# Kernel tuning notes

Hardware: AMD Instinct MI355X
Metric: run time of the kernel (lower is better)

## Reference

```python
import jax, jax.numpy as jnp
import numpy as np

N_NODES = 100000
N_EDGES = 1000000
D = 64
HID = 64
OUT = 64
N_CLS = 10
N_GRAPHS = 512
BN_EPS = 1e-5


def setup_inputs() -> dict:
    key = jax.random.key(0)
    ks = jax.random.split(key, 16)
    inp = {
        "x": jax.random.normal(ks[0], (N_NODES, D), dtype=jnp.float32),
        "edge_index": jax.random.randint(ks[1], (2, N_EDGES), 0, N_NODES, dtype=jnp.int32),
        "batch": jnp.sort(jax.random.randint(ks[2], (N_NODES,), 0, N_GRAPHS, dtype=jnp.int32)),
    }
    def lin(k, fi, fo):
        lim = 1.0 / np.sqrt(fi)
        kw, kb = jax.random.split(k)
        return (jax.random.uniform(kw, (fi, fo), minval=-lim, maxval=lim, dtype=jnp.float32),
                jax.random.uniform(kb, (fo,), minval=-lim, maxval=lim, dtype=jnp.float32))
    # conv0 MLP([64,64,64]) with BN after first linear
    inp["w0a"], inp["b0a"] = lin(ks[3], D, HID)
    inp["g0"] = jnp.ones((HID,), jnp.float32); inp["be0"] = jnp.zeros((HID,), jnp.float32)
    inp["m0"] = jnp.zeros((HID,), jnp.float32); inp["v0"] = jnp.ones((HID,), jnp.float32)
    inp["w0b"], inp["b0b"] = lin(ks[4], HID, HID)
    # conv1 MLP([64,64,64])
    inp["w1a"], inp["b1a"] = lin(ks[5], HID, HID)
    inp["g1"] = jnp.ones((HID,), jnp.float32); inp["be1"] = jnp.zeros((HID,), jnp.float32)
    inp["m1"] = jnp.zeros((HID,), jnp.float32); inp["v1"] = jnp.ones((HID,), jnp.float32)
    inp["w1b"], inp["b1b"] = lin(ks[6], HID, OUT)
    # classifier
    inp["wc"], inp["bc"] = lin(ks[7], OUT, N_CLS)
    return inp


def _bn_eval(h, g, b, m, v):
    return (h - m) * jax.lax.rsqrt(v + BN_EPS) * g + b


def _mlp(h, wa, ba, g, be, m, v, wb, bb):
    # Linear -> BN -> ReLU -> (dropout eval=identity) -> Linear
    h = h @ wa + ba
    h = jax.nn.relu(_bn_eval(h, g, be, m, v))
    return h @ wb + bb


def _gin_conv(h, src, dst, wa, ba, g, be, m, v, wb, bb):
    # GINConv eps=0: mlp(x + sum_{j->i} x_j), messages scatter-added at dst
    agg = jax.ops.segment_sum(h[src], dst, num_segments=N_NODES)
    return _mlp(h + agg, wa, ba, g, be, m, v, wb, bb)


def reference(x, edge_index, batch,
              w0a, b0a, g0, be0, m0, v0, w0b, b0b,
              w1a, b1a, g1, be1, m1, v1, w1b, b1b,
              wc, bc):
    src, dst = edge_index[0], edge_index[1]
    h = _gin_conv(x, src, dst, w0a, b0a, g0, be0, m0, v0, w0b, b0b)
    h = jax.nn.relu(h)  # dropout is identity in eval
    h = _gin_conv(h, src, dst, w1a, b1a, g1, be1, m1, v1, w1b, b1b)
    # global mean pool over batch indices
    sums = jax.ops.segment_sum(h, batch, num_segments=N_GRAPHS)
    cnts = jax.ops.segment_sum(jnp.ones((h.shape[0],), h.dtype), batch, num_segments=N_GRAPHS)
    pooled = sums / jnp.maximum(cnts, 1.0)[:, None]
    return pooled @ wc + bc
```

## Files before the change

kernel.cpp:

```cpp
#include <hip/hip_runtime.h>

#define N_NODES 100000
#define N_EDGES 1000000
#define N_GRAPHS 512
#define N_CLS 10
#define BN_EPS 1e-5f

#define SCAN_NB 200
#define NTILES2 3125

typedef _Float16 half8 __attribute__((ext_vector_type(8)));
typedef _Float16 half4v __attribute__((ext_vector_type(4)));
typedef float floatx4 __attribute__((ext_vector_type(4)));

__global__ __launch_bounds__(256) void prep_kernel(
    const float* __restrict__ x, _Float16* __restrict__ xh,
    const int* __restrict__ batch, const int* __restrict__ dstI,
    int* __restrict__ deg, int* __restrict__ rank,
    const float* __restrict__ w0a, const float* __restrict__ b0a,
    const float* __restrict__ g0, const float* __restrict__ be0,
    const float* __restrict__ m0, const float* __restrict__ v0,
    const float* __restrict__ w0b,
    const float* __restrict__ w1a, const float* __restrict__ b1a,
    const float* __restrict__ g1, const float* __restrict__ be1,
    const float* __restrict__ m1, const float* __restrict__ v1,
    const float* __restrict__ w1b,
    int* __restrict__ gstart,
    _Float16* __restrict__ wHi, _Float16* __restrict__ wLo,
    float* __restrict__ b1p0, float* __restrict__ b1p1) {
    const int gid = blockIdx.x * 256 + threadIdx.x;

    if (gid < 1600000) {
        float4 v = ((const float4*)x)[gid];
        half4v h = {(_Float16)v.x, (_Float16)v.y, (_Float16)v.z, (_Float16)v.w};
        ((half4v*)xh)[gid] = h;
    }

    if (gid < N_EDGES)
        rank[gid] = atomicAdd(&deg[dstI[gid]], 1);

    if (gid <= N_NODES) {
        int bcur = (gid < N_NODES) ? batch[gid] : N_GRAPHS;
        int bprev = (gid > 0) ? batch[gid - 1] : -1;
        for (int g = bprev + 1; g <= bcur; ++g) gstart[g] = gid;
    }

    if (gid < 16384) {
        const int e = gid & 4095, mat = gid >> 12;
        const int jj = e & 7, lane = (e >> 3) & 63, c = (e >> 9) & 3, k0 = (e >> 11) & 1;
        const int k = k0 * 32 + (lane >> 4) * 8 + jj;
        const int col = c * 16 + (lane & 15);
        float val;
        if (mat == 0)      val = w0a[k * 64 + col] * (rsqrtf(v0[col] + BN_EPS) * g0[col]);
        else if (mat == 1) val = w0b[k * 64 + col];
        else if (mat == 2) val = w1a[k * 64 + col] * (rsqrtf(v1[col] + BN_EPS) * g1[col]);
        else               val = w1b[k * 64 + col];
        _Float16 hi = (_Float16)val;
        wHi[gid] = hi;
        wLo[gid] = (_Float16)(val - (float)hi);
    }

    if (gid >= 16384 && gid < 16512) {
        int t = gid - 16384;
        if (t < 64) {
            float s = rsqrtf(v0[t] + BN_EPS) * g0[t];
            b1p0[t] = (b0a[t] - m0[t]) * s + be0[t];
        } else {
            t -= 64;
            float s = rsqrtf(v1[t] + BN_EPS) * g1[t];
            b1p1[t] = (b1a[t] - m1[t]) * s + be1[t];
        }
    }
}

__global__ __launch_bounds__(256) void scanA_kernel(const int* __restrict__ deg,
                                                    int* __restrict__ bsum) {
    __shared__ int sh[256];
    const int base = blockIdx.x * 512;
    const int t = threadIdx.x;
    int a = 0, b = 0;
    if (base + t < N_NODES) a = deg[base + t];
    if (base + 256 + t < N_NODES) b = deg[base + 256 + t];
    sh[t] = a + b;
    __syncthreads();
#pragma unroll
    for (int off = 128; off > 0; off >>= 1) {
        if (t < off) sh[t] += sh[t + off];
        __syncthreads();
    }
    if (t == 0) bsum[blockIdx.x] = sh[0];
}

__global__ __launch_bounds__(256) void scanC_kernel(const int* __restrict__ deg,
                                                    const int* __restrict__ bsum,
                                                    int* __restrict__ rowptr) {
    __shared__ int sh[256];
    __shared__ int sboff[256];
    const int base = blockIdx.x * 512;
    const int t = threadIdx.x;

    const int bv = (t < SCAN_NB) ? bsum[t] : 0;
    sboff[t] = bv;

    const int i0 = base + 2 * t, i1 = i0 + 1;
    const int d0 = (i0 < N_NODES) ? deg[i0] : 0;
    const int d1 = (i1 < N_NODES) ? deg[i1] : 0;
    const int p = d0 + d1;
    sh[t] = p;
    __syncthreads();
#pragma unroll
    for (int off = 1; off < 256; off <<= 1) {
        int u = (t >= off) ? sh[t - off] : 0;
        int ub = (t >= off) ? sboff[t - off] : 0;
        __syncthreads();
        sh[t] += u;
        sboff[t] += ub;
        __syncthreads();
    }
    const int myoff = (blockIdx.x == 0) ? 0 : sboff[blockIdx.x - 1];
    const int excl = myoff + sh[t] - p;
    if (i0 < N_NODES) rowptr[i0] = excl;
    if (i1 < N_NODES) rowptr[i1] = excl + d0;
    if (blockIdx.x == 0 && t == 0) rowptr[N_NODES] = N_EDGES;
}

__global__ __launch_bounds__(256) void fill_kernel(const int* __restrict__ srcI,
                                                   const int* __restrict__ dstI,
                                                   const int* __restrict__ rank,
                                                   const int* __restrict__ rowptr,
                                                   int* __restrict__ sortedSrc) {
    int e = blockIdx.x * 256 + threadIdx.x;
    if (e >= N_EDGES) return;
    sortedSrc[rowptr[dstI[e]] + rank[e]] = srcI[e];
}

template <int POOL>
__global__ __launch_bounds__(128) void conv_mfma(
    const _Float16* __restrict__ in, const int* __restrict__ rowptr,
    const int* __restrict__ srcList,
    const _Float16* __restrict__ wH1, const _Float16* __restrict__ wL1,
    const _Float16* __restrict__ wH2, const _Float16* __restrict__ wL2,
    const float* __restrict__ b1, const float* __restrict__ b2,
    _Float16* __restrict__ out, const int* __restrict__ batch,
    float* __restrict__ pooled) {
    __shared__ __align__(16) _Float16 scratch[2][2304];
    __shared__ float pooledLoc[8 * 64];
    __shared__ int bIds[32];
    __shared__ int maxSlot;

    const int tid = threadIdx.x;
    const int j = tid & 63, wv = tid >> 6;
    const int eoff = j >> 4;
    const int lf = j & 15;
    const int base = blockIdx.x * 32;
    const int strip0 = base + wv * 16;

    if (POOL) {
#pragma unroll
        for (int q = 0; q < 4; ++q) pooledLoc[tid + q * 128] = 0.f;
        if (tid == 0) maxSlot = 0;
        if (j < 16) bIds[wv * 16 + j] = batch[strip0 + j];
    }

    const int rpv = rowptr[strip0 + min(j, 16)];

    _Float16* aggH = scratch[wv];
    _Float16* aggL = scratch[wv] + 1152;

    for (int mq = 0; mq < 4; ++mq) {
        const int m0 = mq * 4;
        int rr[5];
#pragma unroll
        for (int i = 0; i < 5; ++i) rr[i] = __builtin_amdgcn_readlane(rpv, m0 + i);
        int cnt[4];
#pragma unroll
        for (int i = 0; i < 4; ++i) cnt[i] = rr[i + 1] - rr[i];

        float aR[4][4];
#pragma unroll
        for (int i = 0; i < 4; ++i)
#pragma unroll
            for (int q = 0; q < 4; ++q) aR[i][q] = 0.f;

        half4v sS[4];
#pragma unroll
        for (int i = 0; i < 4; ++i) {
            sS[i] = (half4v){0, 0, 0, 0};
            if (eoff == 0)
                sS[i] = *(const half4v*)(in + (size_t)(strip0 + m0 + i) * 64 + lf * 4);
        }
        half4v vT[4][4];
#pragma unroll
        for (int i = 0; i < 4; ++i) {
            const int g = (min(cnt[i], 16) + 3) >> 2;
#pragma unroll
            for (int k = 0; k < 4; ++k) {
                vT[i][k] = (half4v){0, 0, 0, 0};
                if (k < g) {
                    int ec = min(4 * k + eoff, cnt[i] - 1);
                    int id = srcList[rr[i] + ec];
                    vT[i][k] = *(const half4v*)(in + (size_t)id * 64 + lf * 4);
                }
            }
        }
#pragma unroll
        for (int i = 0; i < 4; ++i) {
#pragma unroll
            for (int k = 0; k < 4; ++k) {
                if (4 * k + eoff < cnt[i]) {
                    aR[i][0] += (float)vT[i][k].x; aR[i][1] += (float)vT[i][k].y;
                    aR[i][2] += (float)vT[i][k].z; aR[i][3] += (float)vT[i][k].w;
                }
            }
        }
#pragma unroll
        for (int i = 0; i < 4; ++i) {
            for (int eb = 16; eb < cnt[i]; eb += 16) {
#pragma unroll
                for (int k = 0; k < 4; ++k) {
                    int e_ = eb + 4 * k + eoff;
                    if (e_ < cnt[i]) {
                        int id = srcList[rr[i] + e_];
                        half4v t = *(const half4v*)(in + (size_t)id * 64 + lf * 4);
                        aR[i][0] += (float)t.x; aR[i][1] += (float)t.y;
                        aR[i][2] += (float)t.z; aR[i][3] += (float)t.w;
                    }
                }
            }
        }
#pragma unroll
        for (int i = 0; i < 4; ++i) {
            if (eoff == 0) {
                aR[i][0] += (float)sS[i].x; aR[i][1] += (float)sS[i].y;
                aR[i][2] += (float)sS[i].z; aR[i][3] += (float)sS[i].w;
            }
#pragma unroll
            for (int q = 0; q < 4; ++q) {
                aR[i][q] += __shfl_xor(aR[i][q], 16, 64);
                aR[i][q] += __shfl_xor(aR[i][q], 32, 64);
            }
            if (j < 16) {
                half4v hi, lo;
#pragma unroll
                for (int q = 0; q < 4; ++q) {
                    hi[q] = (_Float16)aR[i][q];
                    lo[q] = (_Float16)(aR[i][q] - (float)hi[q]);
                }
                *(half4v*)(aggH + (m0 + i) * 72 + 4 * j) = hi;
                *(half4v*)(aggL + (m0 + i) * 72 + 4 * j) = lo;
            }
        }
    }

    const int l15 = j & 15, quad = j >> 4;
    const floatx4 vzero = {0.f, 0.f, 0.f, 0.f};

    floatx4 acc[4] = {vzero, vzero, vzero, vzero};
    {
        const _Float16* aH0 = aggH + l15 * 72 + quad * 8;
        const _Float16* aL0 = aggL + l15 * 72 + quad * 8;
#pragma unroll
        for (int k0 = 0; k0 < 2; ++k0) {
            half8 aH = *(const half8*)(aH0 + k0 * 32);
            half8 aL = *(const half8*)(aL0 + k0 * 32);
#pragma unroll
            for (int c = 0; c < 4; ++c) {
                const int fo = ((k0 * 4 + c) * 64 + j) * 8;
                half8 bH = *(const half8*)(wH1 + fo);
                half8 bL = *(const half8*)(wL1 + fo);
                acc[c] = __builtin_amdgcn_mfma_f32_16x16x32_f16(aH, bH, acc[c], 0, 0, 0);
                acc[c] = __builtin_amdgcn_mfma_f32_16x16x32_f16(aL, bH, acc[c], 0, 0, 0);
                acc[c] = __builtin_amdgcn_mfma_f32_16x16x32_f16(aH, bL, acc[c], 0, 0, 0);
            }
        }
    }
    _Float16* hH = aggH;
    _Float16* hL = aggL;
#pragma unroll
    for (int c = 0; c < 4; ++c) {
        const float bv = b1[c * 16 + l15];
#pragma unroll
        for (int r = 0; r < 4; ++r) {
            const int row = quad * 4 + r, col = c * 16 + l15;
            float v = acc[c][r] + bv;
            v = fmaxf(v, 0.f);
            const _Float16 hi = (_Float16)v;
            hH[row * 72 + col] = hi;
            hL[row * 72 + col] = (_Float16)(v - (float)hi);
        }
    }

    floatx4 acc2[4] = {vzero, vzero, vzero, vzero};
    {
        const _Float16* aH0 = hH + l15 * 72 + quad * 8;
        const _Float16* aL0 = hL + l15 * 72 + quad * 8;
#pragma unroll
        for (int k0 = 0; k0 < 2; ++k0) {
            half8 aH = *(const half8*)(aH0 + k0 * 32);
            half8 aL = *(const half8*)(aL0 + k0 * 32);
#pragma unroll
            for (int c = 0; c < 4; ++c) {
                const int fo = ((k0 * 4 + c) * 64 + j) * 8;
                half8 bH = *(const half8*)(wH2 + fo);
                half8 bL = *(const half8*)(wL2 + fo);
                acc2[c] = __builtin_amdgcn_mfma_f32_16x16x32_f16(aH, bH, acc2[c], 0, 0, 0);
                acc2[c] = __builtin_amdgcn_mfma_f32_16x16x32_f16(aL, bH, acc2[c], 0, 0, 0);
                acc2[c] = __builtin_amdgcn_mfma_f32_16x16x32_f16(aH, bL, acc2[c], 0, 0, 0);
            }
        }
    }

    if (!POOL) {
#pragma unroll
        for (int c = 0; c < 4; ++c) {
            const float bv = b2[c * 16 + l15];
#pragma unroll
            for (int r = 0; r < 4; ++r) {
                const int node = strip0 + quad * 4 + r;
                out[(size_t)node * 64 + c * 16 + l15] =
                    (_Float16)fmaxf(acc2[c][r] + bv, 0.f);
            }
        }
    } else {
        float* oT = (float*)scratch[wv];
#pragma unroll
        for (int c = 0; c < 4; ++c) {
            const float bv = b2[c * 16 + l15];
#pragma unroll
            for (int r = 0; r < 4; ++r)
                oT[(quad * 4 + r) * 66 + c * 16 + l15] = acc2[c][r] + bv;
        }
        __syncthreads();
        const int b0 = bIds[0];
        int curB = -1;
        float accv = 0.f;
        for (int r = 0; r < 16; ++r) {
            const int b = bIds[wv * 16 + r];
            const float v = oT[r * 66 + j];
            if (b != curB) {
                if (curB >= 0) {
                    const int s = curB - b0;
                    if (s >= 0 && s < 8) {
                        atomicAdd(&pooledLoc[s * 64 + j], accv);
                        if (j == 0) atomicMax(&maxSlot, s);
                    } else {
                        atomicAdd(&pooled[curB * 64 + j], accv);
                    }
                }
                curB = b;
                accv = v;
            } else {
                accv += v;
            }
        }
        {
            const int s = curB - b0;
            if (s >= 0 && s < 8) {
                atomicAdd(&pooledLoc[s * 64 + j], accv);
                if (j == 0) atomicMax(&maxSlot, s);
            } else {
                atomicAdd(&pooled[curB * 64 + j], accv);
            }
        }
        __syncthreads();
        const int ns = maxSlot + 1;
        for (int s = wv; s < ns; s += 2)
            atomicAdd(&pooled[(b0 + s) * 64 + j], pooledLoc[s * 64 + j]);
    }
}

__global__ __launch_bounds__(64) void classifier_kernel(const float* __restrict__ pooled,
                                                        const int* __restrict__ gstart,
                                                        const float* __restrict__ wc,
                                                        const float* __restrict__ bc,
                                                        float* __restrict__ out) {
    const int g = blockIdx.x;
    const int j = threadIdx.x;
    const float c = fmaxf((float)(gstart[g + 1] - gstart[g]), 1.f);
    const float mean = pooled[g * 64 + j] / c;
#pragma unroll
    for (int cc = 0; cc < N_CLS; ++cc) {
        float p = mean * wc[j * N_CLS + cc];
#pragma unroll
        for (int off = 32; off > 0; off >>= 1) p += __shfl_down(p, off, 64);
        if (j == 0) out[g * N_CLS + cc] = p + bc[cc];
    }
}


extern "C" void kernel_launch(void* const* d_in, const int* in_sizes, int n_in,
                              void* d_out, int out_size, void* d_ws, size_t ws_size,
                              hipStream_t stream) {
    const float* x   = (const float*)d_in[0];
    const int*   ei  = (const int*)d_in[1];
    const int* batch = (const int*)d_in[2];
    const float* w0a = (const float*)d_in[3];
    const float* b0a = (const float*)d_in[4];
    const float* g0  = (const float*)d_in[5];
    const float* be0 = (const float*)d_in[6];
    const float* m0  = (const float*)d_in[7];
    const float* v0  = (const float*)d_in[8];
    const float* w0b = (const float*)d_in[9];
    const float* b0b = (const float*)d_in[10];
    const float* w1a = (const float*)d_in[11];
    const float* b1a = (const float*)d_in[12];
    const float* g1  = (const float*)d_in[13];
    const float* be1 = (const float*)d_in[14];
    const float* m1  = (const float*)d_in[15];
    const float* v1  = (const float*)d_in[16];
    const float* w1b = (const float*)d_in[17];
    const float* b1b = (const float*)d_in[18];
    const float* wc  = (const float*)d_in[19];
    const float* bc  = (const float*)d_in[20];
    float* out = (float*)d_out;

    const int* srcI = ei;
    const int* dstI = ei + N_EDGES;

    int* ws = (int*)d_ws;
    int*      deg       = ws;
    int*      bsum      = ws + 100000;
    float*    pooled    = (float*)(ws + 100404);
    int*      rowptr    = ws + 133172;
    int*      rank      = ws + 233176;
    int*      sortedSrc = ws + 1233176;
    _Float16* xh        = (_Float16*)(ws + 2233176);
    _Float16* h1        = (_Float16*)(ws + 5433176);
    float*    b1p0      = (float*)(ws + 8633176);
    float*    b1p1      = (float*)(ws + 8633240);
    int*      gstart    = ws + 8633304;
    _Float16* wHi       = (_Float16*)(ws + 8633820);
    _Float16* wLo       = (_Float16*)(ws + 8642012);

    (void)hipMemsetAsync((void*)deg, 0, 133172 * sizeof(int), stream);
    prep_kernel<<<6250, 256, 0, stream>>>(x, xh, batch, dstI, deg, rank,
                                          w0a, b0a, g0, be0, m0, v0, w0b,
                                          w1a, b1a, g1, be1, m1, v1, w1b,
                                          gstart, wHi, wLo, b1p0, b1p1);

    scanA_kernel<<<SCAN_NB, 256, 0, stream>>>(deg, bsum);
    scanC_kernel<<<SCAN_NB, 256, 0, stream>>>(deg, bsum, rowptr);
    fill_kernel<<<(N_EDGES + 255) / 256, 256, 0, stream>>>(srcI, dstI, rank, rowptr, sortedSrc);

    conv_mfma<0><<<NTILES2, 128, 0, stream>>>(xh, rowptr, sortedSrc,
                                              wHi, wLo, wHi + 4096, wLo + 4096,
                                              b1p0, b0b, h1, nullptr, nullptr);

    conv_mfma<1><<<NTILES2, 128, 0, stream>>>(h1, rowptr, sortedSrc,
                                              wHi + 8192, wLo + 8192, wHi + 12288, wLo + 12288,
                                              b1p1, b1b, nullptr, batch, pooled);

    classifier_kernel<<<N_GRAPHS, 64, 0, stream>>>(pooled, gstart, wc, bc, out);
}
```

Baseline: 292.0 us.

## Merge CSR build stages into one cooperative kernel with grid syncs

```diff
diff --git a/kernel.cpp b/kernel.cpp
--- a/kernel.cpp
+++ b/kernel.cpp
@@ -1,4 +1,5 @@
 #include <hip/hip_runtime.h>
+#include <hip/hip_cooperative_groups.h>
 
 #define N_NODES 100000
 #define N_EDGES 1000000
@@ -6,16 +7,19 @@
 #define N_CLS 10
 #define BN_EPS 1e-5f
 
-#define SCAN_NB 200
 #define NTILES2 3125
+#define CB 512
+#define CCHUNK 196
+#define ZN 133172
 
 typedef _Float16 half8 __attribute__((ext_vector_type(8)));
 typedef _Float16 half4v __attribute__((ext_vector_type(4)));
 typedef float floatx4 __attribute__((ext_vector_type(4)));
 
-__global__ __launch_bounds__(256) void prep_kernel(
+__global__ __launch_bounds__(256) void build_kernel(
     const float* __restrict__ x, _Float16* __restrict__ xh,
-    const int* __restrict__ batch, const int* __restrict__ dstI,
+    const int* __restrict__ batch, const int* __restrict__ srcI,
+    const int* __restrict__ dstI,
     int* __restrict__ deg, int* __restrict__ rank,
     const float* __restrict__ w0a, const float* __restrict__ b0a,
     const float* __restrict__ g0, const float* __restrict__ be0,
@@ -27,24 +31,32 @@
     const float* __restrict__ w1b,
     int* __restrict__ gstart,
     _Float16* __restrict__ wHi, _Float16* __restrict__ wLo,
-    float* __restrict__ b1p0, float* __restrict__ b1p1) {
-    const int gid = blockIdx.x * 256 + threadIdx.x;
-
-    if (gid < 1600000) {
-        float4 v = ((const float4*)x)[gid];
+    float* __restrict__ b1p0, float* __restrict__ b1p1,
+    int* __restrict__ bsum, int* __restrict__ boff,
+    int* __restrict__ rowptr, int* __restrict__ sortedSrc) {
+    cooperative_groups::grid_group grid = cooperative_groups::this_grid();
+    __shared__ int sh[256];
+
+    const int t = threadIdx.x;
+    const int blk = blockIdx.x;
+    const int gid = blk * 256 + t;
+    const int stride = CB * 256;
+
+    for (int i = gid; i < ZN; i += stride) deg[i] = 0;
+    grid.sync();
+
+    for (int i = gid; i < 1600000; i += stride) {
+        float4 v = ((const float4*)x)[i];
         half4v h = {(_Float16)v.x, (_Float16)v.y, (_Float16)v.z, (_Float16)v.w};
-        ((half4v*)xh)[gid] = h;
-    }
-
-    if (gid < N_EDGES)
-        rank[gid] = atomicAdd(&deg[dstI[gid]], 1);
-
-    if (gid <= N_NODES) {
-        int bcur = (gid < N_NODES) ? batch[gid] : N_GRAPHS;
-        int bprev = (gid > 0) ? batch[gid - 1] : -1;
-        for (int g = bprev + 1; g <= bcur; ++g) gstart[g] = gid;
-    }
-
+        ((half4v*)xh)[i] = h;
+    }
+    for (int e = gid; e < N_EDGES; e += stride)
+        rank[e] = atomicAdd(&deg[dstI[e]], 1);
+    for (int i = gid; i <= N_NODES; i += stride) {
+        int bcur = (i < N_NODES) ? batch[i] : N_GRAPHS;
+        int bprev = (i > 0) ? batch[i - 1] : -1;
+        for (int g = bprev + 1; g <= bcur; ++g) gstart[g] = i;
+    }
     if (gid < 16384) {
         const int e = gid & 4095, mat = gid >> 12;
         const int jj = e & 7, lane = (e >> 3) & 63, c = (e >> 9) & 3, k0 = (e >> 11) & 1;
@@ -59,79 +71,68 @@
         wHi[gid] = hi;
         wLo[gid] = (_Float16)(val - (float)hi);
     }
-
     if (gid >= 16384 && gid < 16512) {
-        int t = gid - 16384;
-        if (t < 64) {
-            float s = rsqrtf(v0[t] + BN_EPS) * g0[t];
-            b1p0[t] = (b0a[t] - m0[t]) * s + be0[t];
+        int tt = gid - 16384;
+        if (tt < 64) {
+            float s = rsqrtf(v0[tt] + BN_EPS) * g0[tt];
+            b1p0[tt] = (b0a[tt] - m0[tt]) * s + be0[tt];
         } else {
-            t -= 64;
-            float s = rsqrtf(v1[t] + BN_EPS) * g1[t];
-            b1p1[t] = (b1a[t] - m1[t]) * s + be1[t];
-        }
-    }
-}
-
-__global__ __launch_bounds__(256) void scanA_kernel(const int* __restrict__ deg,
-                                                    int* __restrict__ bsum) {
-    __shared__ int sh[256];
-    const int base = blockIdx.x * 512;
-    const int t = threadIdx.x;
-    int a = 0, b = 0;
-    if (base + t < N_NODES) a = deg[base + t];
-    if (base + 256 + t < N_NODES) b = deg[base + 256 + t];
-    sh[t] = a + b;
-    __syncthreads();
-#pragma unroll
-    for (int off = 128; off > 0; off >>= 1) {
-        if (t < off) sh[t] += sh[t + off];
+            tt -= 64;
+            float s = rsqrtf(v1[tt] + BN_EPS) * g1[tt];
+            b1p1[tt] = (b1a[tt] - m1[tt]) * s + be1[tt];
+        }
+    }
+    grid.sync();
+
+    {
+        const int idx = blk * CCHUNK + t;
+        sh[t] = (t < CCHUNK && idx < N_NODES) ? deg[idx] : 0;
         __syncthreads();
-    }
-    if (t == 0) bsum[blockIdx.x] = sh[0];
-}
-
-__global__ __launch_bounds__(256) void scanC_kernel(const int* __restrict__ deg,
-                                                    const int* __restrict__ bsum,
-                                                    int* __restrict__ rowptr) {
-    __shared__ int sh[256];
-    __shared__ int sboff[256];
-    const int base = blockIdx.x * 512;
-    const int t = threadIdx.x;
-
-    const int bv = (t < SCAN_NB) ? bsum[t] : 0;
-    sboff[t] = bv;
-
-    const int i0 = base + 2 * t, i1 = i0 + 1;
-    const int d0 = (i0 < N_NODES) ? deg[i0] : 0;
-    const int d1 = (i1 < N_NODES) ? deg[i1] : 0;
-    const int p = d0 + d1;
-    sh[t] = p;
-    __syncthreads();
-#pragma unroll
-    for (int off = 1; off < 256; off <<= 1) {
-        int u = (t >= off) ? sh[t - off] : 0;
-        int ub = (t >= off) ? sboff[t - off] : 0;
+#pragma unroll
+        for (int off = 128; off > 0; off >>= 1) {
+            if (t < off) sh[t] += sh[t + off];
+            __syncthreads();
+        }
+        if (t == 0) bsum[blk] = sh[0];
+    }
+    grid.sync();
+
+    if (blk == 0) {
+        const int a = bsum[2 * t], b = bsum[2 * t + 1];
+        sh[t] = a + b;
         __syncthreads();
-        sh[t] += u;
-        sboff[t] += ub;
+#pragma unroll
+        for (int off = 1; off < 256; off <<= 1) {
+            int u = (t >= off) ? sh[t - off] : 0;
+            __syncthreads();
+            sh[t] += u;
+            __syncthreads();
+        }
+        const int exclPair = sh[t] - (a + b);
+        boff[2 * t] = exclPair;
+        boff[2 * t + 1] = exclPair + a;
+    }
+    grid.sync();
+
+    {
+        const int idx = blk * CCHUNK + t;
+        const int v = (t < CCHUNK && idx < N_NODES) ? deg[idx] : 0;
+        sh[t] = v;
         __syncthreads();
-    }
-    const int myoff = (blockIdx.x == 0) ? 0 : sboff[blockIdx.x - 1];
-    const int excl = myoff + sh[t] - p;
-    if (i0 < N_NODES) rowptr[i0] = excl;
-    if (i1 < N_NODES) rowptr[i1] = excl + d0;
-    if (blockIdx.x == 0 && t == 0) rowptr[N_NODES] = N_EDGES;
-}
-
-__global__ __launch_bounds__(256) void fill_kernel(const int* __restrict__ srcI,
-                                                   const int* __restrict__ dstI,
-                                                   const int* __restrict__ rank,
-                                                   const int* __restrict__ rowptr,
-                                                   int* __restrict__ sortedSrc) {
-    int e = blockIdx.x * 256 + threadIdx.x;
-    if (e >= N_EDGES) return;
-    sortedSrc[rowptr[dstI[e]] + rank[e]] = srcI[e];
+#pragma unroll
+        for (int off = 1; off < 256; off <<= 1) {
+            int u = (t >= off) ? sh[t - off] : 0;
+            __syncthreads();
+            sh[t] += u;
+            __syncthreads();
+        }
+        if (t < CCHUNK && idx < N_NODES) rowptr[idx] = boff[blk] + sh[t] - v;
+        if (blk == 0 && t == 0) rowptr[N_NODES] = N_EDGES;
+    }
+    grid.sync();
+
+    for (int e = gid; e < N_EDGES; e += stride)
+        sortedSrc[rowptr[dstI[e]] + rank[e]] = srcI[e];
 }
 
 template <int POOL>
@@ -221,9 +222,9 @@
                     int e_ = eb + 4 * k + eoff;
                     if (e_ < cnt[i]) {
                         int id = srcList[rr[i] + e_];
-                        half4v t = *(const half4v*)(in + (size_t)id * 64 + lf * 4);
-                        aR[i][0] += (float)t.x; aR[i][1] += (float)t.y;
-                        aR[i][2] += (float)t.z; aR[i][3] += (float)t.w;
+                        half4v tv = *(const half4v*)(in + (size_t)id * 64 + lf * 4);
+                        aR[i][0] += (float)tv.x; aR[i][1] += (float)tv.y;
+                        aR[i][2] += (float)tv.z; aR[i][3] += (float)tv.w;
                     }
                 }
             }
@@ -420,27 +421,30 @@
     int* ws = (int*)d_ws;
     int*      deg       = ws;
     int*      bsum      = ws + 100000;
-    float*    pooled    = (float*)(ws + 100404);
-    int*      rowptr    = ws + 133172;
-    int*      rank      = ws + 233176;
-    int*      sortedSrc = ws + 1233176;
-    _Float16* xh        = (_Float16*)(ws + 2233176);
-    _Float16* h1        = (_Float16*)(ws + 5433176);
-    float*    b1p0      = (float*)(ws + 8633176);
-    float*    b1p1      = (float*)(ws + 8633240);
-    int*      gstart    = ws + 8633304;
-    _Float16* wHi       = (_Float16*)(ws + 8633820);
-    _Float16* wLo       = (_Float16*)(ws + 8642012);
-
-    (void)hipMemsetAsync((void*)deg, 0, 133172 * sizeof(int), stream);
-    prep_kernel<<<6250, 256, 0, stream>>>(x, xh, batch, dstI, deg, rank,
-                                          w0a, b0a, g0, be0, m0, v0, w0b,
-                                          w1a, b1a, g1, be1, m1, v1, w1b,
-                                          gstart, wHi, wLo, b1p0, b1p1);
-
-    scanA_kernel<<<SCAN_NB, 256, 0, stream>>>(deg, bsum);
-    scanC_kernel<<<SCAN_NB, 256, 0, stream>>>(deg, bsum, rowptr);
-    fill_kernel<<<(N_EDGES + 255) / 256, 256, 0, stream>>>(srcI, dstI, rank, rowptr, sortedSrc);
+    float*    pooled    = (float*)(ws + 100516);
+    int*      boff      = ws + 133284;
+    int*      rowptr    = ws + 133800;
+    int*      rank      = ws + 233804;
+    int*      sortedSrc = ws + 1233804;
+    _Float16* xh        = (_Float16*)(ws + 2233804);
+    _Float16* h1        = (_Float16*)(ws + 5433804);
+    float*    b1p0      = (float*)(ws + 8633804);
+    float*    b1p1      = (float*)(ws + 8633868);
+    int*      gstart    = ws + 8633932;
+    _Float16* wHi       = (_Float16*)(ws + 8634448);
+    _Float16* wLo       = (_Float16*)(ws + 8642640);
+
+    void* args[] = {
+        (void*)&x, (void*)&xh, (void*)&batch, (void*)&srcI, (void*)&dstI,
+        (void*)&deg, (void*)&rank,
+        (void*)&w0a, (void*)&b0a, (void*)&g0, (void*)&be0, (void*)&m0, (void*)&v0,
+        (void*)&w0b,
+        (void*)&w1a, (void*)&b1a, (void*)&g1, (void*)&be1, (void*)&m1, (void*)&v1,
+        (void*)&w1b,
+        (void*)&gstart, (void*)&wHi, (void*)&wLo, (void*)&b1p0, (void*)&b1p1,
+        (void*)&bsum, (void*)&boff, (void*)&rowptr, (void*)&sortedSrc};
+    (void)hipLaunchCooperativeKernel((void*)build_kernel, dim3(CB), dim3(256),
+                                     args, 0, stream);
 
     conv_mfma<0><<<NTILES2, 128, 0, stream>>>(xh, rowptr, sortedSrc,
                                               wHi, wLo, wHi + 4096, wLo + 4096,
```

Measured after the change: 578.4 us. 98.1% more time.
